# Optimization experiments

Measured on AMD Instinct MI355X. Metric: run time of the kernel, lower is better.

## Reference

```python
import jax, jax.numpy as jnp
import numpy as np

B, IN_SHAPE, EXP_SHAPE, HID, NB_CLASSES = 64, 10000, 53, 1500, 2048


def setup_inputs() -> dict:
    key = jax.random.key(0)
    ks = jax.random.split(key, 8)
    gos = jax.random.uniform(ks[0], (B, IN_SHAPE), dtype=jnp.float32)
    exp_x = jax.random.uniform(ks[1], (B, EXP_SHAPE), dtype=jnp.float32)
    # FlatModel params (torch Linear: y = x @ W.T + b; store pre-transposed)
    W1 = jax.random.normal(ks[2], (IN_SHAPE, HID), dtype=jnp.float32) * (1.0 / np.sqrt(IN_SHAPE))
    b1 = jnp.zeros((HID,), dtype=jnp.float32)
    W2 = jax.random.normal(ks[3], (HID + EXP_SHAPE, NB_CLASSES), dtype=jnp.float32) * (1.0 / np.sqrt(HID + EXP_SHAPE))
    b2 = jnp.zeros((NB_CLASSES,), dtype=jnp.float32)
    # HPO adjacency (non-trainable buffer in the original; values in [0,1))
    hpo_matrix = jax.random.uniform(ks[4], (NB_CLASSES, NB_CLASSES), dtype=jnp.float32)
    return {"gos": gos, "exp_x": exp_x, "W1": W1, "b1": b1, "W2": W2, "b2": b2, "hpo_matrix": hpo_matrix}


def reference(gos, exp_x, W1, b1, W2, b2, hpo_matrix):
    # FlatModel (eval mode: dropout is identity). torch F.gelu default = exact erf gelu.
    h = jax.nn.gelu(gos @ W1 + b1, approximate=False)          # (B, HID)
    x = jnp.concatenate([h, exp_x], axis=1)                     # (B, HID+EXP)
    flat = jax.nn.sigmoid(x @ W2 + b2)                          # (B, C)
    # HPOLayer + permute + MaxPool1d(C): out[b,j] = max_i flat[b,j] * M[i,j]
    out = jnp.max(flat[:, None, :] * hpo_matrix[None, :, :], axis=1)  # (B, C)
    return out
```

## Files before the change

### kernel.cpp

```cpp
#include <hip/hip_runtime.h>
#include <math.h>

#define B64 64
#define IN_SH 10000
#define EXP_SH 53
#define HID 1500
#define NPAD1 1536
#define NBC 2048
#define K2 1553
#define KS1 40
#define KST1 8
#define KS2 13
#define KST2 4
#define NSTEP1 320
#define NSTEP2 52
#define CMCH 32

using short8  = __attribute__((ext_vector_type(8))) short;
using floatx4 = __attribute__((ext_vector_type(4))) float;
using uintx4  = __attribute__((ext_vector_type(4))) unsigned int;

__device__ __forceinline__ unsigned short f2bf(float f) {
    unsigned u = __float_as_uint(f);
    u += 0x7fffu + ((u >> 16) & 1u);
    return (unsigned short)(u >> 16);
}


__global__ __launch_bounds__(256) void prep_k(const float* __restrict__ g,
                                              unsigned short* __restrict__ gosBf,
                                              const float* __restrict__ M,
                                              float* __restrict__ cm,
                                              float* __restrict__ accz) {
    int bi = blockIdx.x;
    if (bi < 320) {
        int t    = bi * 256 + threadIdx.x;
        int lane = t & 63;
        int sgrp = (t >> 6) & 3;
        int step = t >> 8;
        int q    = lane >> 4;
        int l15  = lane & 15;
        int b    = sgrp * 16 + l15;
        int k0   = step * 32 + q * 8;
        const float* p = g + (size_t)b * IN_SH + k0;
        unsigned int o[4];
        #pragma unroll
        for (int i = 0; i < 4; i++) {
            float lo = (k0 + 2 * i     < IN_SH) ? p[2 * i]     : 0.f;
            float hi = (k0 + 2 * i + 1 < IN_SH) ? p[2 * i + 1] : 0.f;
            o[i] = (unsigned)f2bf(lo) | ((unsigned)f2bf(hi) << 16);
        }
        uintx4 v; v.x = o[0]; v.y = o[1]; v.z = o[2]; v.w = o[3];
        *(uintx4*)(gosBf + (size_t)t * 8) = v;
    } else if (bi < 576) {
        int ci = bi - 320;
        int j  = (ci & 7) * 256 + threadIdx.x;
        int i0 = (ci >> 3) * 64;
        float m = 0.0f;
        #pragma unroll 16
        for (int i = i0; i < i0 + 64; i++)
            m = fmaxf(m, M[(size_t)i * NBC + j]);
        cm[(ci >> 3) * NBC + j] = m;
    } else {
        int t = (bi - 576) * 256 + threadIdx.x;
        floatx4 z = (floatx4){0.f, 0.f, 0.f, 0.f};
        #pragma unroll
        for (int i = 0; i < 28; i++)
            *(floatx4*)(accz + (size_t)(i * 2048 + t) * 4) = z;
    }
}

__device__ __forceinline__ void load_w8(const float* __restrict__ W, int kb, int K,
                                        int ldw, int cW, bool nok, float wv[8]) {
    #pragma unroll
    for (int j = 0; j < 8; j++) {
        int k = kb + j;
        wv[j] = (nok && k < K) ? W[(size_t)k * ldw + cW] : 0.f;
    }
}
__device__ __forceinline__ void load_b4(const unsigned short* __restrict__ bf,
                                        int stg, uintx4 bv[4]) {
    #pragma unroll
    for (int s = 0; s < 4; s++)
        bv[s] = *(const uintx4*)(bf + (size_t)(stg * 4 + s) * 512);
}

template<int KSTEPS>
__device__ __forceinline__ void gemm_core(
    const float* __restrict__ W, const unsigned short* __restrict__ Bf,
    float* __restrict__ accbuf, int N, int K, int ldw, int bx, int by, int tid)
{
    int w    = tid >> 6;
    int lane = tid & 63;
    int q    = lane >> 4;
    int l15  = lane & 15;
    int n0   = bx * 64;
    int k0   = by * (KSTEPS * 32);
    int cW   = n0 + 16 * w + l15;
    bool nok = cW < N;
    int qk   = q * 8;

    const unsigned short* bf = Bf + (size_t)(by * KSTEPS * 4) * 512 + (size_t)lane * 8;

    floatx4 acc[4];
    #pragma unroll
    for (int s = 0; s < 4; s++) acc[s] = (floatx4){0.f, 0.f, 0.f, 0.f};

    float  wv[3][8];
    uintx4 bv[3][4];
    #pragma unroll
    for (int d = 0; d < 3; d++) {
        int st = (d < KSTEPS) ? d : KSTEPS - 1;
        load_w8(W, k0 + st * 32 + qk, K, ldw, cW, nok, wv[d]);
        load_b4(bf, st, bv[d]);
    }

    #pragma unroll
    for (int st = 0; st < KSTEPS; st++) {
        const int p = st % 3;
        float  wt[8];
        uintx4 bt[4];
        if (st + 3 < KSTEPS) {
            load_w8(W, k0 + (st + 3) * 32 + qk, K, ldw, cW, nok, wt);
            load_b4(bf, st + 3, bt);
        }

        short8 af;
        #pragma unroll
        for (int j = 0; j < 8; j++) af[j] = (short)f2bf(wv[p][j]);
        #pragma unroll
        for (int s = 0; s < 4; s++) {
            short8 bf8 = __builtin_bit_cast(short8, bv[p][s]);
            acc[s] = __builtin_amdgcn_mfma_f32_16x16x32_bf16(af, bf8, acc[s], 0, 0, 0);
        }

        if (st + 3 < KSTEPS) {
            #pragma unroll
            for (int j = 0; j < 8; j++) wv[p][j] = wt[j];
            #pragma unroll
            for (int s = 0; s < 4; s++) bv[p][s] = bt[s];
        }
    }

    int nrow = n0 + 16 * w + q * 4;
    #pragma unroll
    for (int s = 0; s < 4; s++) {
        #pragma unroll
        for (int r = 0; r < 4; r++)
            atomicAdd(&accbuf[(size_t)(nrow + r) * 64 + s * 16 + l15], acc[s][r]);
    }
}

__global__ __launch_bounds__(256) void gemm1_k(
    const float* __restrict__ W1, const unsigned short* __restrict__ gosBf,
    float* __restrict__ hpre)
{
    gemm_core<KST1>(W1, gosBf, hpre, HID, IN_SH, HID, blockIdx.x, blockIdx.y, threadIdx.x);
}

__global__ __launch_bounds__(256) void gemm2_k(
    const float* __restrict__ W2, const unsigned short* __restrict__ Xf,
    float* __restrict__ logits)
{
    gemm_core<KST2>(W2, Xf, logits, NBC, K2, NBC, blockIdx.x, blockIdx.y, threadIdx.x);
}

__global__ __launch_bounds__(256) void combine1(
    const float* __restrict__ hpre, const float* __restrict__ b1,
    const float* __restrict__ expx, unsigned short* __restrict__ Xf)
{
    int t    = blockIdx.x * 256 + threadIdx.x;
    int lane = t & 63;
    int sgrp = (t >> 6) & 3;
    int step = t >> 8;
    int q    = lane >> 4;
    int l15  = lane & 15;
    int b    = sgrp * 16 + l15;
    int kb   = step * 32 + q * 8;
    unsigned int o[4];
    #pragma unroll
    for (int i = 0; i < 4; i++) {
        unsigned int lohi[2];
        #pragma unroll
        for (int h = 0; h < 2; h++) {
            int n = kb + 2 * i + h;
            float v = 0.f;
            if (n < HID) {
                float s = hpre[(size_t)n * 64 + b] + b1[n];
                v = 0.5f * s * (1.0f + erff(s * 0.70710678118654752f));
            } else if (n < HID + EXP_SH) {
                v = expx[b * EXP_SH + (n - HID)];
            }
            lohi[h] = f2bf(v);
        }
        o[i] = lohi[0] | (lohi[1] << 16);
    }
    uintx4 v; v.x = o[0]; v.y = o[1]; v.z = o[2]; v.w = o[3];
    *(uintx4*)(Xf + (size_t)t * 8) = v;
}

__global__ __launch_bounds__(256) void final_k(
    const float* __restrict__ logits, const float* __restrict__ b2,
    const float* __restrict__ cm, float* __restrict__ out)
{
    int idx = blockIdx.x * 256 + threadIdx.x;
    int b = idx & 63;
    int j = idx >> 6;
    float s = logits[(size_t)j * 64 + b] + b2[j];
    float sig = 1.0f / (1.0f + expf(-s));
    float m = 0.f;
    #pragma unroll
    for (int c = 0; c < CMCH; c++) m = fmaxf(m, cm[c * NBC + j]);
    out[(size_t)b * NBC + j] = sig * m;
}

extern "C" void kernel_launch(void* const* d_in, const int* in_sizes, int n_in,
                              void* d_out, int out_size, void* d_ws, size_t ws_size,
                              hipStream_t stream) {
    const float* gos  = (const float*)d_in[0];
    const float* expx = (const float*)d_in[1];
    const float* W1   = (const float*)d_in[2];
    const float* b1   = (const float*)d_in[3];
    const float* W2   = (const float*)d_in[4];
    const float* b2   = (const float*)d_in[5];
    const float* hpo  = (const float*)d_in[6];
    float* out = (float*)d_out;

    char* ws = (char*)d_ws;
    unsigned short* gosBf = (unsigned short*)ws;
    float* hpre   = (float*)(ws + 1310720);
    float* logits = (float*)(ws + 1310720 + 393216);
    unsigned short* Xf = (unsigned short*)(ws + 1310720 + 393216 + 524288);
    float* cm = (float*)(ws + 1310720 + 393216 + 524288 + 212992);

    prep_k<<<584, 256, 0, stream>>>(gos, gosBf, hpo, cm, hpre);

    gemm1_k<<<dim3(NPAD1 / 64, KS1), 256, 0, stream>>>(W1, gosBf, hpre);

    combine1<<<52, 256, 0, stream>>>(hpre, b1, expx, Xf);

    gemm2_k<<<dim3(NBC / 64, KS2), 256, 0, stream>>>(W2, Xf, logits);

    final_k<<<(B64 * NBC) / 256, 256, 0, stream>>>(logits, b2, cm, out);
}
```

Baseline: 162.7 us.

## Stage weight tiles through double-buffered LDS using vectorized float4 global loads

Replaces per-lane strided scalar weight loads in both GEMMs with cooperative float4 row loads into a double-buffered shared-memory tile. Each lane then reads its column-strided A fragment from LDS, using a padded stride of 65 to limit bank conflicts. The goal is wider, better-coalesced global reads of W1/W2 with fewer load instructions. The cost is a __syncthreads per k-step, a shallower register prefetch (one stage ahead instead of three) and float4 LDS stores at addresses that are not 16-byte aligned for odd rows.

```diff
diff --git a/kernel.cpp b/kernel.cpp
--- a/kernel.cpp
+++ b/kernel.cpp
@@ -12,9 +12,8 @@
 #define KST1 8
 #define KS2 13
 #define KST2 4
-#define NSTEP1 320
-#define NSTEP2 52
 #define CMCH 32
+#define LDSF 2080
 
 using short8  = __attribute__((ext_vector_type(8))) short;
 using floatx4 = __attribute__((ext_vector_type(4))) float;
@@ -70,25 +69,49 @@
     }
 }
 
-__device__ __forceinline__ void load_w8(const float* __restrict__ W, int kb, int K,
-                                        int ldw, int cW, bool nok, float wv[8]) {
-    #pragma unroll
-    for (int j = 0; j < 8; j++) {
-        int k = kb + j;
-        wv[j] = (nok && k < K) ? W[(size_t)k * ldw + cW] : 0.f;
-    }
-}
 __device__ __forceinline__ void load_b4(const unsigned short* __restrict__ bf,
                                         int stg, uintx4 bv[4]) {
     #pragma unroll
     for (int s = 0; s < 4; s++)
         bv[s] = *(const uintx4*)(bf + (size_t)(stg * 4 + s) * 512);
+}
+
+__device__ __forceinline__ void stage_load(
+    const float* __restrict__ W, int kg0, int n0, int N, int K, int ldw,
+    int tid, bool fast, float r[2][4])
+{
+    #pragma unroll
+    for (int i = 0; i < 2; i++) {
+        int kl = (tid >> 4) + 16 * i;
+        int kg = kg0 + kl;
+        int n  = n0 + (tid & 15) * 4;
+        if (fast) {
+            floatx4 v = *(const floatx4*)(W + (size_t)kg * ldw + n);
+            r[i][0] = v.x; r[i][1] = v.y; r[i][2] = v.z; r[i][3] = v.w;
+        } else {
+            #pragma unroll
+            for (int j = 0; j < 4; j++)
+                r[i][j] = (kg < K && n + j < N) ? W[(size_t)kg * ldw + n + j] : 0.f;
+        }
+    }
+}
+
+__device__ __forceinline__ void stage_write(float* __restrict__ ldsb, int tid,
+                                            const float r[2][4]) {
+    #pragma unroll
+    for (int i = 0; i < 2; i++) {
+        int kl  = (tid >> 4) + 16 * i;
+        int seg = tid & 15;
+        floatx4 v; v.x = r[i][0]; v.y = r[i][1]; v.z = r[i][2]; v.w = r[i][3];
+        *(floatx4*)(ldsb + kl * 65 + seg * 4) = v;
+    }
 }
 
 template<int KSTEPS>
 __device__ __forceinline__ void gemm_core(
     const float* __restrict__ W, const unsigned short* __restrict__ Bf,
-    float* __restrict__ accbuf, int N, int K, int ldw, int bx, int by, int tid)
+    float* __restrict__ accbuf, int N, int K, int ldw, int bx, int by, int tid,
+    float (*lds)[LDSF])
 {
     int w    = tid >> 6;
     int lane = tid & 63;
@@ -96,9 +119,7 @@
     int l15  = lane & 15;
     int n0   = bx * 64;
     int k0   = by * (KSTEPS * 32);
-    int cW   = n0 + 16 * w + l15;
-    bool nok = cW < N;
-    int qk   = q * 8;
+    bool fast = (n0 + 64 <= N) && (k0 + KSTEPS * 32 <= K);
 
     const unsigned short* bf = Bf + (size_t)(by * KSTEPS * 4) * 512 + (size_t)lane * 8;
 
@@ -106,37 +127,39 @@
     #pragma unroll
     for (int s = 0; s < 4; s++) acc[s] = (floatx4){0.f, 0.f, 0.f, 0.f};
 
-    float  wv[3][8];
-    uintx4 bv[3][4];
-    #pragma unroll
-    for (int d = 0; d < 3; d++) {
-        int st = (d < KSTEPS) ? d : KSTEPS - 1;
-        load_w8(W, k0 + st * 32 + qk, K, ldw, cW, nok, wv[d]);
-        load_b4(bf, st, bv[d]);
-    }
+    float r[2][4];
+    stage_load(W, k0, n0, N, K, ldw, tid, fast, r);
+    stage_write(lds[0], tid, r);
+
+    uintx4 bv[2][4];
+    load_b4(bf, 0, bv[0]);
+    if (KSTEPS > 1) load_b4(bf, 1, bv[1]);
 
     #pragma unroll
     for (int st = 0; st < KSTEPS; st++) {
-        const int p = st % 3;
-        float  wt[8];
+        if (st + 1 < KSTEPS)
+            stage_load(W, k0 + (st + 1) * 32, n0, N, K, ldw, tid, fast, r);
         uintx4 bt[4];
-        if (st + 3 < KSTEPS) {
-            load_w8(W, k0 + (st + 3) * 32 + qk, K, ldw, cW, nok, wt);
-            load_b4(bf, st + 3, bt);
-        }
-
+        if (st + 2 < KSTEPS) load_b4(bf, st + 2, bt);
+
+        __syncthreads();
+
+        const float* lb = lds[st & 1];
         short8 af;
         #pragma unroll
-        for (int j = 0; j < 8; j++) af[j] = (short)f2bf(wv[p][j]);
+        for (int j = 0; j < 8; j++)
+            af[j] = (short)f2bf(lb[(q * 8 + j) * 65 + 16 * w + l15]);
+
+        const int p = st & 1;
         #pragma unroll
         for (int s = 0; s < 4; s++) {
             short8 bf8 = __builtin_bit_cast(short8, bv[p][s]);
             acc[s] = __builtin_amdgcn_mfma_f32_16x16x32_bf16(af, bf8, acc[s], 0, 0, 0);
         }
 
-        if (st + 3 < KSTEPS) {
-            #pragma unroll
-            for (int j = 0; j < 8; j++) wv[p][j] = wt[j];
+        if (st + 1 < KSTEPS)
+            stage_write(lds[(st + 1) & 1], tid, r);
+        if (st + 2 < KSTEPS) {
             #pragma unroll
             for (int s = 0; s < 4; s++) bv[p][s] = bt[s];
         }
@@ -146,8 +169,8 @@
     #pragma unroll
     for (int s = 0; s < 4; s++) {
         #pragma unroll
-        for (int r = 0; r < 4; r++)
-            atomicAdd(&accbuf[(size_t)(nrow + r) * 64 + s * 16 + l15], acc[s][r]);
+        for (int rr = 0; rr < 4; rr++)
+            atomicAdd(&accbuf[(size_t)(nrow + rr) * 64 + s * 16 + l15], acc[s][rr]);
     }
 }
 
@@ -155,14 +178,18 @@
     const float* __restrict__ W1, const unsigned short* __restrict__ gosBf,
     float* __restrict__ hpre)
 {
-    gemm_core<KST1>(W1, gosBf, hpre, HID, IN_SH, HID, blockIdx.x, blockIdx.y, threadIdx.x);
+    __shared__ float lds[2][LDSF];
+    gemm_core<KST1>(W1, gosBf, hpre, HID, IN_SH, HID, blockIdx.x, blockIdx.y,
+                    threadIdx.x, lds);
 }
 
 __global__ __launch_bounds__(256) void gemm2_k(
     const float* __restrict__ W2, const unsigned short* __restrict__ Xf,
     float* __restrict__ logits)
 {
-    gemm_core<KST2>(W2, Xf, logits, NBC, K2, NBC, blockIdx.x, blockIdx.y, threadIdx.x);
+    __shared__ float lds[2][LDSF];
+    gemm_core<KST2>(W2, Xf, logits, NBC, K2, NBC, blockIdx.x, blockIdx.y,
+                    threadIdx.x, lds);
 }
 
 __global__ __launch_bounds__(256) void combine1(
```

After: 162.4 us. About the same (-0.2%).

## Stage weight tiles through per-wave LDS with vectorized float4 global loads

Applied to the files above, without the earlier changes.

Weight loads in both GEMMs change from eight scalar strided column reads per lane to row-contiguous float4 loads, which are written into a per-wave double-buffered LDS tile (padded stride 20) and read back transposed into the MFMA A-fragment layout. The prefetch depth drops from three stages to two. The aim is fewer global load instructions and better coalescing on the bandwidth-bound weight stream. In exchange it adds LDS traffic, 20KB of shared memory per block, and relies on in-wave ordering between LDS writes and reads without any explicit barrier.

```diff
diff --git a/kernel.cpp b/kernel.cpp
--- a/kernel.cpp
+++ b/kernel.cpp
@@ -12,9 +12,8 @@
 #define KST1 8
 #define KS2 13
 #define KST2 4
-#define NSTEP1 320
-#define NSTEP2 52
 #define CMCH 32
+#define WLDS 640
 
 using short8  = __attribute__((ext_vector_type(8))) short;
 using floatx4 = __attribute__((ext_vector_type(4))) float;
@@ -70,14 +69,6 @@
     }
 }
 
-__device__ __forceinline__ void load_w8(const float* __restrict__ W, int kb, int K,
-                                        int ldw, int cW, bool nok, float wv[8]) {
-    #pragma unroll
-    for (int j = 0; j < 8; j++) {
-        int k = kb + j;
-        wv[j] = (nok && k < K) ? W[(size_t)k * ldw + cW] : 0.f;
-    }
-}
 __device__ __forceinline__ void load_b4(const unsigned short* __restrict__ bf,
                                         int stg, uintx4 bv[4]) {
     #pragma unroll
@@ -88,17 +79,17 @@
 template<int KSTEPS>
 __device__ __forceinline__ void gemm_core(
     const float* __restrict__ W, const unsigned short* __restrict__ Bf,
-    float* __restrict__ accbuf, int N, int K, int ldw, int bx, int by, int tid)
-{
-    int w    = tid >> 6;
+    float* __restrict__ accbuf, int N, int K, int ldw, int bx, int by, int tid,
+    float* __restrict__ ldsw)
+{
     int lane = tid & 63;
     int q    = lane >> 4;
     int l15  = lane & 15;
-    int n0   = bx * 64;
+    int n0   = bx * 64 + 16 * (tid >> 6);
     int k0   = by * (KSTEPS * 32);
-    int cW   = n0 + 16 * w + l15;
-    bool nok = cW < N;
-    int qk   = q * 8;
+    bool fast = (n0 + 16 <= N) && (k0 + KSTEPS * 32 <= K);
+    int kl  = lane >> 2;
+    int c4  = (lane & 3) * 4;
 
     const unsigned short* bf = Bf + (size_t)(by * KSTEPS * 4) * 512 + (size_t)lane * 8;
 
@@ -106,48 +97,76 @@
     #pragma unroll
     for (int s = 0; s < 4; s++) acc[s] = (floatx4){0.f, 0.f, 0.f, 0.f};
 
-    float  wv[3][8];
-    uintx4 bv[3][4];
-    #pragma unroll
-    for (int d = 0; d < 3; d++) {
-        int st = (d < KSTEPS) ? d : KSTEPS - 1;
-        load_w8(W, k0 + st * 32 + qk, K, ldw, cW, nok, wv[d]);
-        load_b4(bf, st, bv[d]);
-    }
+    floatx4 g[2][2];
+
+    #define GLB(st, slot)                                                        \
+        {                                                                        \
+            int kb_ = k0 + (st) * 32;                                            \
+            _Pragma("unroll")                                                    \
+            for (int i_ = 0; i_ < 2; i_++) {                                     \
+                int kg_ = kb_ + kl + 16 * i_;                                    \
+                if (fast) {                                                      \
+                    g[slot][i_] = *(const floatx4*)(W + (size_t)kg_ * ldw + n0 + c4); \
+                } else {                                                         \
+                    _Pragma("unroll")                                            \
+                    for (int j_ = 0; j_ < 4; j_++)                               \
+                        g[slot][i_][j_] = (kg_ < K && n0 + c4 + j_ < N)          \
+                            ? W[(size_t)kg_ * ldw + n0 + c4 + j_] : 0.f;         \
+                }                                                                \
+            }                                                                    \
+        }
+    #define LWR(buf, slot)                                                       \
+        {                                                                        \
+            _Pragma("unroll")                                                    \
+            for (int i_ = 0; i_ < 2; i_++)                                       \
+                *(floatx4*)(ldsw + (buf) * WLDS + (kl + 16 * i_) * 20 + c4) = g[slot][i_]; \
+        }
+
+    GLB(0, 0);
+    if (KSTEPS > 1) GLB(1, 1);
+    LWR(0, 0);
+
+    uintx4 bv[2][4];
+    load_b4(bf, 0, bv[0]);
+    if (KSTEPS > 1) load_b4(bf, 1, bv[1]);
 
     #pragma unroll
     for (int st = 0; st < KSTEPS; st++) {
-        const int p = st % 3;
-        float  wt[8];
+        const int s = st & 1;
+        const float* lb = ldsw + s * WLDS;
+
+        short8 af;
+        #pragma unroll
+        for (int j = 0; j < 8; j++)
+            af[j] = (short)f2bf(lb[(q * 8 + j) * 20 + l15]);
+
         uintx4 bt[4];
-        if (st + 3 < KSTEPS) {
-            load_w8(W, k0 + (st + 3) * 32 + qk, K, ldw, cW, nok, wt);
-            load_b4(bf, st + 3, bt);
-        }
-
-        short8 af;
-        #pragma unroll
-        for (int j = 0; j < 8; j++) af[j] = (short)f2bf(wv[p][j]);
-        #pragma unroll
-        for (int s = 0; s < 4; s++) {
-            short8 bf8 = __builtin_bit_cast(short8, bv[p][s]);
-            acc[s] = __builtin_amdgcn_mfma_f32_16x16x32_bf16(af, bf8, acc[s], 0, 0, 0);
-        }
-
-        if (st + 3 < KSTEPS) {
+        if (st + 2 < KSTEPS) {
+            GLB(st + 2, s);
+            load_b4(bf, st + 2, bt);
+        }
+
+        #pragma unroll
+        for (int m = 0; m < 4; m++) {
+            short8 bf8 = __builtin_bit_cast(short8, bv[s][m]);
+            acc[m] = __builtin_amdgcn_mfma_f32_16x16x32_bf16(af, bf8, acc[m], 0, 0, 0);
+        }
+
+        if (st + 1 < KSTEPS) LWR(1 - s, 1 - s);
+        if (st + 2 < KSTEPS) {
             #pragma unroll
-            for (int j = 0; j < 8; j++) wv[p][j] = wt[j];
-            #pragma unroll
-            for (int s = 0; s < 4; s++) bv[p][s] = bt[s];
-        }
-    }
-
-    int nrow = n0 + 16 * w + q * 4;
+            for (int m = 0; m < 4; m++) bv[s][m] = bt[m];
+        }
+    }
+    #undef GLB
+    #undef LWR
+
+    int nrow = n0 + q * 4;
     #pragma unroll
     for (int s = 0; s < 4; s++) {
         #pragma unroll
-        for (int r = 0; r < 4; r++)
-            atomicAdd(&accbuf[(size_t)(nrow + r) * 64 + s * 16 + l15], acc[s][r]);
+        for (int rr = 0; rr < 4; rr++)
+            atomicAdd(&accbuf[(size_t)(nrow + rr) * 64 + s * 16 + l15], acc[s][rr]);
     }
 }
 
@@ -155,14 +174,18 @@
     const float* __restrict__ W1, const unsigned short* __restrict__ gosBf,
     float* __restrict__ hpre)
 {
-    gemm_core<KST1>(W1, gosBf, hpre, HID, IN_SH, HID, blockIdx.x, blockIdx.y, threadIdx.x);
+    __shared__ float lds[4 * 2 * WLDS];
+    gemm_core<KST1>(W1, gosBf, hpre, HID, IN_SH, HID, blockIdx.x, blockIdx.y,
+                    threadIdx.x, lds + (threadIdx.x >> 6) * (2 * WLDS));
 }
 
 __global__ __launch_bounds__(256) void gemm2_k(
     const float* __restrict__ W2, const unsigned short* __restrict__ Xf,
     float* __restrict__ logits)
 {
-    gemm_core<KST2>(W2, Xf, logits, NBC, K2, NBC, blockIdx.x, blockIdx.y, threadIdx.x);
+    __shared__ float lds[4 * 2 * WLDS];
+    gemm_core<KST2>(W2, Xf, logits, NBC, K2, NBC, blockIdx.x, blockIdx.y,
+                    threadIdx.x, lds + (threadIdx.x >> 6) * (2 * WLDS));
 }
 
 __global__ __launch_bounds__(256) void combine1(
```

Measured after the change: 162.3 us. No clear change (-0.2%).
